# Kernel optimization log

Measured on AMD Instinct MI355X. Metric: run time of the kernel, lower is better.

The kernel has to match this reference:

```python
import jax, jax.numpy as jnp
import numpy as np

B, S, D, H = 4, 2048, 1024, 16
HD = D // H
DFF = 4 * D
NUM_LAYERS = 12
RES = 1.0 / float(np.sqrt(NUM_LAYERS))
SCALE = 1.0 / float(np.sqrt(D))  # module divides by sqrt(embed_dim), not head_dim
EPS = 1e-5


def setup_inputs() -> dict:
    key = jax.random.key(0)
    ks = jax.random.split(key, 12)
    s = 0.02
    p = lambda k, shp: (jax.random.normal(k, shp, jnp.float32) * s)
    return {
        "x": jax.random.normal(ks[0], (B, S, D), jnp.float32),
        "Wq": p(ks[1], (D, D)), "bq": jnp.zeros((D,), jnp.float32),
        "Wk": p(ks[2], (D, D)), "bk": jnp.zeros((D,), jnp.float32),
        "Wv": p(ks[3], (D, D)), "bv": jnp.zeros((D,), jnp.float32),
        "Wo": p(ks[4], (D, D)), "bo": jnp.zeros((D,), jnp.float32),
        "g1": jnp.ones((D,), jnp.float32), "be1": jnp.zeros((D,), jnp.float32),
        "g2": jnp.ones((D,), jnp.float32), "be2": jnp.zeros((D,), jnp.float32),
        "W1": p(ks[5], (D, DFF)), "b1": jnp.zeros((DFF,), jnp.float32),
        "W2": p(ks[6], (DFF, D)), "b2": jnp.zeros((D,), jnp.float32),
    }


def _layernorm(x, g, b):
    m = jnp.mean(x, axis=-1, keepdims=True)
    v = jnp.mean((x - m) ** 2, axis=-1, keepdims=True)
    return (x - m) * jax.lax.rsqrt(v + EPS) * g + b


def _attention(x, Wq, bq, Wk, bk, Wv, bv, Wo, bo):
    b, s, d = x.shape
    q = (x @ Wq + bq).reshape(b, s, H, HD)
    k = (x @ Wk + bk).reshape(b, s, H, HD)
    v = (x @ Wv + bv).reshape(b, s, H, HD)
    scores = jnp.einsum('bqhd,bkhd->bhqk', q, k) * SCALE  # [B,H,S,S]
    mask = jnp.tril(jnp.ones((s, s), dtype=bool))
    scores = jnp.where(mask, scores, -jnp.inf)
    attn = jax.nn.softmax(scores, axis=-1)  # dropout_rate=0 -> identity
    out = jnp.einsum('bhqk,bkhd->bqhd', attn, v).reshape(b, s, d)
    return out @ Wo + bo


def reference(x, Wq, bq, Wk, bk, Wv, bv, Wo, bo, g1, be1, g2, be2, W1, b1, W2, b2):
    x = x + RES * _attention(_layernorm(x, g1, be1), Wq, bq, Wk, bk, Wv, bv, Wo, bo)
    h = _layernorm(x, g2, be2)
    ffn = jax.nn.relu(h @ W1 + b1) @ W2 + b2
    x = x + RES * ffn
    return x
```

## Files before the change

### kernel.cpp

```cpp
#include <hip/hip_runtime.h>

typedef unsigned short ushort_t;
typedef unsigned int uint32;
typedef __attribute__((ext_vector_type(4))) float f32x4;
typedef __attribute__((ext_vector_type(8))) short bf16x8;

#define B_   4
#define S_   2048
#define D_   1024
#define H_   16
#define HD_  64
#define DFF_ 4096
#define M_   (B_ * S_)

#define RES_   0.28867513459481287f
#define SCALE_ 0.03125f
#define EPS_   1e-5f
#define LOG2E_ 1.4426950408889634f

__device__ __forceinline__ ushort_t f2bf(float f) {
    union { float f; uint32 u; } c; c.f = f;
    uint32 u = c.u + 0x7fffu + ((c.u >> 16) & 1u);
    return (ushort_t)(u >> 16);
}
__device__ __forceinline__ float bf2f(ushort_t h) {
    union { uint32 u; float f; } c; c.u = ((uint32)h) << 16;
    return c.f;
}
__device__ __forceinline__ float fexp2(float x) {
    float r; asm("v_exp_f32 %0, %1" : "=v"(r) : "v"(x)); return r;
}
__device__ __forceinline__ uint32 cvt_pk_bf16(float lo, float hi) {
    uint32 r;
    asm("v_cvt_pk_bf16_f32 %0, %1, %2" : "=v"(r) : "v"(lo), "v"(hi));
    return r;
}

#define GLDS(src_, dst_)                                                     \
    __builtin_amdgcn_global_load_lds(                                        \
        (const __attribute__((address_space(1))) void*)(src_),               \
        (__attribute__((address_space(3))) void*)(dst_), 16, 0, 0)

__global__ __launch_bounds__(256) void transpose_cast_kernel(
    const float* __restrict__ W, ushort_t* __restrict__ Wt, int K, int N)
{
    __shared__ float tile[32][33];
    const int bx = blockIdx.x * 32;
    const int by = blockIdx.y * 32;
    const int tx = threadIdx.x;
    const int ty = threadIdx.y;
    #pragma unroll
    for (int i = 0; i < 32; i += 8)
        tile[ty + i][tx] = W[(size_t)(by + ty + i) * N + bx + tx];
    __syncthreads();
    #pragma unroll
    for (int i = 0; i < 32; i += 8)
        Wt[(size_t)(bx + ty + i) * K + by + tx] = f2bf(tile[tx][ty + i]);
}

__global__ void concat_bias_kernel(const float* __restrict__ bq,
                                   const float* __restrict__ bk,
                                   const float* __restrict__ bv,
                                   float* __restrict__ bqkv)
{
    int i = blockIdx.x * blockDim.x + threadIdx.x;
    if (i < 3 * D_) {
        float v = (i < D_) ? bq[i] : (i < 2 * D_) ? bk[i - D_] : bv[i - 2 * D_];
        bqkv[i] = v;
    }
}

__global__ __launch_bounds__(256) void ln_kernel(
    const float* __restrict__ x, const float* __restrict__ g,
    const float* __restrict__ be, ushort_t* __restrict__ out)
{
    const int row = blockIdx.x;
    const int t = threadIdx.x;
    const int lane = t & 63;
    const int wave = t >> 6;
    const float4* xr = (const float4*)(x + (size_t)row * D_);
    float4 v = xr[t];
    float s  = v.x + v.y + v.z + v.w;
    float s2 = v.x * v.x + v.y * v.y + v.z * v.z + v.w * v.w;
    #pragma unroll
    for (int off = 32; off; off >>= 1) {
        s  += __shfl_xor(s, off);
        s2 += __shfl_xor(s2, off);
    }
    __shared__ float red[8];
    if (lane == 0) { red[wave * 2] = s; red[wave * 2 + 1] = s2; }
    __syncthreads();
    s  = red[0] + red[2] + red[4] + red[6];
    s2 = red[1] + red[3] + red[5] + red[7];
    const float mean = s * (1.0f / D_);
    const float var  = s2 * (1.0f / D_) - mean * mean;
    const float rstd = rsqrtf(var + EPS_);
    const float4 gv  = ((const float4*)g)[t];
    const float4 bv  = ((const float4*)be)[t];
    ushort_t o[4];
    o[0] = f2bf((v.x - mean) * rstd * gv.x + bv.x);
    o[1] = f2bf((v.y - mean) * rstd * gv.y + bv.y);
    o[2] = f2bf((v.z - mean) * rstd * gv.z + bv.z);
    o[3] = f2bf((v.w - mean) * rstd * gv.w + bv.w);
    *(ushort2*)&out[(size_t)row * D_ + t * 4]     = make_ushort2(o[0], o[1]);
    *(ushort2*)&out[(size_t)row * D_ + t * 4 + 2] = make_ushort2(o[2], o[3]);
}

template <int MODE, int BM>
__global__ __launch_bounds__(512, (BM == 256) ? 1 : 2) void gemmT_kernel(
    const ushort_t* __restrict__ A, const ushort_t* __restrict__ Bt,
    const float* __restrict__ bias, const float* __restrict__ res,
    void* __restrict__ Cout, int M, int N, int K, int gx)
{
    constexpr int MF     = BM / 32;
    constexpr int ALOADS = BM / 128;
    constexpr int LOADS  = ALOADS + 2;

    __shared__ __align__(16) ushort_t As[3][BM * 32];
    __shared__ __align__(16) ushort_t Bs[3][256 * 32];

    const int tid  = threadIdx.x;
    const int w    = tid >> 6;
    const int lane = tid & 63;
    const int l15  = lane & 15;
    const int g    = lane >> 4;

    const int cpx = gridDim.x >> 3;
    const int swz = (blockIdx.x & 7) * cpx + (blockIdx.x >> 3);
    const int bx = swz % gx, by = swz / gx;
    const int m0 = by * BM, n0 = bx * 256;

    const int wm = (w >> 2) * (BM / 2);
    const int wn = (w & 3) * 64;

    const ushort_t* srcA[ALOADS];
    int ldsA[ALOADS];
    const ushort_t* srcB[2];
    int ldsB[2];
    #pragma unroll
    for (int p = 0; p < ALOADS; ++p) {
        const int L = p * 512 + tid;
        const int row = L >> 2;
        srcA[p] = A + (size_t)(m0 + row) * K + (((L & 3) ^ ((row >> 1) & 3)) << 3);
        ldsA[p] = (p * 512 + w * 64) * 8;
    }
    #pragma unroll
    for (int p = 0; p < 2; ++p) {
        const int L = p * 512 + tid;
        const int row = L >> 2;
        srcB[p] = Bt + (size_t)(n0 + row) * K + (((L & 3) ^ ((row >> 1) & 3)) << 3);
        ldsB[p] = (p * 512 + w * 64) * 8;
    }

    #define STAGE_A(koff_, buf_)                                             \
        do { _Pragma("unroll")                                               \
             for (int p = 0; p < ALOADS; ++p)                                \
                 GLDS(srcA[p] + (koff_), &As[buf_][ldsA[p]]); } while (0)
    #define STAGE_B(koff_, buf_)                                             \
        do { _Pragma("unroll")                                               \
             for (int p = 0; p < 2; ++p)                                     \
                 GLDS(srcB[p] + (koff_), &Bs[buf_][ldsB[p]]); } while (0)

    #define LDA(mf_) (*(const bf16x8*)&As[cur][(wm + (mf_) * 16 + l15) * 32 + \
                        ((g ^ (((wm + (mf_) * 16 + l15) >> 1) & 3)) << 3)])
    #define LDB(nf_) (*(const bf16x8*)&Bs[cur][(wn + (nf_) * 16 + l15) * 32 + \
                        ((g ^ (((wn + (nf_) * 16 + l15) >> 1) & 3)) << 3)])

    f32x4 acc[MF][4] = {};
    const int NT = K >> 5;

    STAGE_A(0, 0); STAGE_B(0, 0);
    STAGE_A(32, 1); STAGE_B(32, 1);
    asm volatile("s_waitcnt vmcnt(%0)" :: "n"(LOADS) : "memory");
    __builtin_amdgcn_s_barrier();

    for (int t = 0; t < NT; ++t) {
        const int cur = t % 3;
        const int nb  = (t + 2) % 3;
        const bool more = (t + 2 < NT);
        const size_t koff = (size_t)(t + 2) * 32;

        bf16x8 af[4], bfr[4];
        #pragma unroll
        for (int nf = 0; nf < 4; ++nf) bfr[nf] = LDB(nf);
        #pragma unroll
        for (int mf = 0; mf < 4; ++mf) af[mf] = LDA(mf);

        if (BM == 256) {
            if (more) STAGE_A(koff, nb);
            __builtin_amdgcn_s_barrier();
            __builtin_amdgcn_s_setprio(1);
            #pragma unroll
            for (int mf = 0; mf < 4; ++mf)
                #pragma unroll
                for (int nf = 0; nf < 4; ++nf)
                    acc[mf][nf] = __builtin_amdgcn_mfma_f32_16x16x32_bf16(
                        af[mf], bfr[nf], acc[mf][nf], 0, 0, 0);
            __builtin_amdgcn_s_setprio(0);
            __builtin_amdgcn_s_barrier();

            #pragma unroll
            for (int mf = 0; mf < 4; ++mf) af[mf] = LDA(mf + 4);
            if (more) STAGE_B(koff, nb);
            __builtin_amdgcn_s_barrier();
            __builtin_amdgcn_s_setprio(1);
            #pragma unroll
            for (int mf = 0; mf < 4; ++mf)
                #pragma unroll
                for (int nf = 0; nf < 4; ++nf)
                    acc[(MF == 8 ? mf + 4 : mf)][nf] =
                        __builtin_amdgcn_mfma_f32_16x16x32_bf16(
                            af[mf], bfr[nf], acc[(MF == 8 ? mf + 4 : mf)][nf], 0, 0, 0);
            __builtin_amdgcn_s_setprio(0);
            if (more)
                asm volatile("s_waitcnt vmcnt(%0)" :: "n"(LOADS) : "memory");
            else
                asm volatile("s_waitcnt vmcnt(0)" ::: "memory");
            __builtin_amdgcn_s_barrier();
        } else {
            if (more) { STAGE_A(koff, nb); STAGE_B(koff, nb); }
            __builtin_amdgcn_s_setprio(1);
            #pragma unroll
            for (int mf = 0; mf < 4; ++mf)
                #pragma unroll
                for (int nf = 0; nf < 4; ++nf)
                    acc[mf][nf] = __builtin_amdgcn_mfma_f32_16x16x32_bf16(
                        af[mf], bfr[nf], acc[mf][nf], 0, 0, 0);
            __builtin_amdgcn_s_setprio(0);
            if (more)
                asm volatile("s_waitcnt vmcnt(%0)" :: "n"(LOADS) : "memory");
            else
                asm volatile("s_waitcnt vmcnt(0)" ::: "memory");
            __builtin_amdgcn_s_barrier();
        }
    }
    #undef STAGE_A
    #undef STAGE_B
    #undef LDA
    #undef LDB

    const int rbase = g * 4;
    #pragma unroll
    for (int mf = 0; mf < MF; ++mf) {
        #pragma unroll
        for (int nf = 0; nf < 4; ++nf) {
            const int col = n0 + wn + nf * 16 + l15;
            const float bcol = bias[col];
            #pragma unroll
            for (int r = 0; r < 4; ++r) {
                const int row = m0 + wm + mf * 16 + rbase + r;
                float v = acc[mf][nf][r] + bcol;
                const size_t idx = (size_t)row * N + col;
                if (MODE == 0) {
                    ((ushort_t*)Cout)[idx] = f2bf(v);
                } else if (MODE == 1) {
                    ((ushort_t*)Cout)[idx] = f2bf(fmaxf(v, 0.0f));
                } else {
                    ((float*)Cout)[idx] = res[idx] + RES_ * v;
                }
            }
        }
    }
}

__global__ __launch_bounds__(256) void fattn_kernel(
    const ushort_t* __restrict__ qkv, ushort_t* __restrict__ out)
{
    __shared__ __align__(16) ushort_t Ks[64 * 64];
    __shared__ __align__(16) ushort_t Vt[64 * 64];
    __shared__ __align__(16) ushort_t Ps[4][16 * 64];

    const int tid  = threadIdx.x;
    const int lane = tid & 63;
    const int w    = tid >> 6;
    const int bh = blockIdx.y;
    const int b = bh >> 4, h = bh & 15;

    const int l15 = lane & 15;
    const int g   = lane >> 4;

    const size_t rs = 3 * D_;
    const ushort_t* Qg = qkv + (size_t)b * S_ * rs + h * HD_;
    const ushort_t* Kg = Qg + D_;

    const int skey = tid >> 3;
    const int sc   = tid & 7;

    #pragma unroll
    for (int half = 0; half < 2; ++half) {
        const int qt = half ? blockIdx.x : (S_ / 64 - 1) - blockIdx.x;
        const int q0 = qt * 64;
        const int nkb = qt + 1;

        bf16x8 qf[2];
        {
            const int qrow = q0 + w * 16 + l15;
            #pragma unroll
            for (int kk = 0; kk < 2; ++kk) {
                bf16x8 tq = *(const bf16x8*)(Qg + (size_t)qrow * rs + kk * 32 + g * 8);
                #pragma unroll
                for (int e = 0; e < 8; ++e)
                    tq[e] = (short)f2bf(bf2f((ushort_t)tq[e]) * (SCALE_ * LOG2E_));
                qf[kk] = tq;
            }
        }

        float mrow = -1e30f, lrow = 0.f;
        f32x4 oacc[4] = {};

        bf16x8 kvreg[2], vvreg[2];
        #pragma unroll
        for (int pass = 0; pass < 2; ++pass) {
            const ushort_t* src = Kg + (size_t)(pass * 32 + skey) * rs + sc * 8;
            kvreg[pass] = *(const bf16x8*)src;
            vvreg[pass] = *(const bf16x8*)(src + D_);
        }

        for (int kb = 0; kb < nkb; ++kb) {
            __syncthreads();
            #pragma unroll
            for (int pass = 0; pass < 2; ++pass) {
                const int key = pass * 32 + skey;
                *(bf16x8*)&Ks[key * 64 + ((sc ^ (key & 7)) << 3)] = kvreg[pass];
                #pragma unroll
                for (int j = 0; j < 8; ++j) {
                    const int d  = sc * 8 + j;
                    const int cp = (key >> 3) ^ (d & 7) ^ ((d >> 3) & 7);
                    Vt[d * 64 + (cp << 3) + (key & 7)] = (ushort_t)vvreg[pass][j];
                }
            }
            if (kb + 1 < nkb) {
                #pragma unroll
                for (int pass = 0; pass < 2; ++pass) {
                    const ushort_t* src =
                        Kg + (size_t)((kb + 1) * 64 + pass * 32 + skey) * rs + sc * 8;
                    kvreg[pass] = *(const bf16x8*)src;
                    vvreg[pass] = *(const bf16x8*)(src + D_);
                }
            }
            __syncthreads();

            f32x4 sf[4] = {};
            __builtin_amdgcn_s_setprio(1);
            #pragma unroll
            for (int kk = 0; kk < 2; ++kk) {
                const int cc = kk * 4 + g;
                #pragma unroll
                for (int nf = 0; nf < 4; ++nf) {
                    const int keyr = nf * 16 + l15;
                    bf16x8 kf = *(const bf16x8*)&Ks[keyr * 64 + ((cc ^ (keyr & 7)) << 3)];
                    sf[nf] = __builtin_amdgcn_mfma_f32_16x16x32_bf16(kf, qf[kk], sf[nf], 0, 0, 0);
                }
            }
            __builtin_amdgcn_s_setprio(0);

            if (kb == nkb - 1) {
                const int q = q0 + w * 16 + l15;
                #pragma unroll
                for (int nf = 0; nf < 4; ++nf)
                    #pragma unroll
                    for (int r = 0; r < 4; ++r)
                        if (kb * 64 + nf * 16 + g * 4 + r > q) sf[nf][r] = -1e30f;
            }
            float mx = -1e30f;
            #pragma unroll
            for (int nf = 0; nf < 4; ++nf)
                #pragma unroll
                for (int r = 0; r < 4; ++r) mx = fmaxf(mx, sf[nf][r]);
            mx = fmaxf(mx, __shfl_xor(mx, 16));
            mx = fmaxf(mx, __shfl_xor(mx, 32));

            if (!__all(mx - mrow <= 8.0f)) {
                const float mnew = fmaxf(mrow, mx);
                const float corr = fexp2(mrow - mnew);
                mrow = mnew;
                lrow *= corr;
                #pragma unroll
                for (int r = 0; r < 4; ++r) {
                    const float cr = __shfl(corr, g * 4 + r, 16);
                    #pragma unroll
                    for (int nf = 0; nf < 4; ++nf) oacc[nf][r] *= cr;
                }
            }

            {
                const int qrow = l15;
                float psum = 0.f;
                #pragma unroll
                for (int nf = 0; nf < 4; ++nf) {
                    const float p0 = fexp2(sf[nf][0] - mrow);
                    const float p1 = fexp2(sf[nf][1] - mrow);
                    const float p2 = fexp2(sf[nf][2] - mrow);
                    const float p3 = fexp2(sf[nf][3] - mrow);
                    psum += (p0 + p1) + (p2 + p3);
                    uint2 pk = make_uint2(cvt_pk_bf16(p0, p1), cvt_pk_bf16(p2, p3));
                    const int c16 = ((nf << 1) + (g >> 1)) ^ (qrow & 7);
                    *(uint2*)((char*)Ps[w] + qrow * 128 + c16 * 16 + (g & 1) * 8) = pk;
                }
                psum += __shfl_xor(psum, 16);
                psum += __shfl_xor(psum, 32);
                lrow += psum;
            }

            #pragma unroll
            for (int kk = 0; kk < 2; ++kk) {
                const int cc = kk * 4 + g;
                const int qrow = l15;
                const int c16 = cc ^ (qrow & 7);
                bf16x8 pa = *(const bf16x8*)((const char*)Ps[w] + qrow * 128 + c16 * 16);
                __builtin_amdgcn_s_setprio(1);
                #pragma unroll
                for (int nf = 0; nf < 4; ++nf) {
                    const int dr  = nf * 16 + l15;
                    const int cvp = cc ^ (dr & 7) ^ ((dr >> 3) & 7);
                    bf16x8 vf = *(const bf16x8*)&Vt[dr * 64 + (cvp << 3)];
                    oacc[nf] = __builtin_amdgcn_mfma_f32_16x16x32_bf16(pa, vf, oacc[nf], 0, 0, 0);
                }
                __builtin_amdgcn_s_setprio(0);
            }
        }

        const float linv = 1.0f / lrow;
        #pragma unroll
        for (int r = 0; r < 4; ++r) {
            const float li = __shfl(linv, g * 4 + r, 16);
            const int q = q0 + w * 16 + g * 4 + r;
            ushort_t* op = out + (size_t)(b * S_ + q) * D_ + h * HD_;
            #pragma unroll
            for (int nf = 0; nf < 4; ++nf)
                op[nf * 16 + l15] = f2bf(oacc[nf][r] * li);
        }
    }
}

extern "C" void kernel_launch(void* const* d_in, const int* in_sizes, int n_in,
                              void* d_out, int out_size, void* d_ws, size_t ws_size,
                              hipStream_t stream)
{
    const float* x   = (const float*)d_in[0];
    const float* Wq  = (const float*)d_in[1];
    const float* bq  = (const float*)d_in[2];
    const float* Wk  = (const float*)d_in[3];
    const float* bk  = (const float*)d_in[4];
    const float* Wv  = (const float*)d_in[5];
    const float* bv  = (const float*)d_in[6];
    const float* Wo  = (const float*)d_in[7];
    const float* bo  = (const float*)d_in[8];
    const float* g1  = (const float*)d_in[9];
    const float* be1 = (const float*)d_in[10];
    const float* g2  = (const float*)d_in[11];
    const float* be2 = (const float*)d_in[12];
    const float* W1  = (const float*)d_in[13];
    const float* b1  = (const float*)d_in[14];
    const float* W2  = (const float*)d_in[15];
    const float* b2  = (const float*)d_in[16];
    float* out = (float*)d_out;

    char* ws = (char*)d_ws;
    size_t o = 0;
    auto alloc = [&](size_t bytes) { size_t r = o; o = (o + bytes + 255) & ~(size_t)255; return r; };
    ushort_t* Wqkvt = (ushort_t*)(ws + alloc((size_t)3 * D_ * D_ * 2));
    ushort_t* Wot   = (ushort_t*)(ws + alloc((size_t)D_ * D_ * 2));
    ushort_t* W1t   = (ushort_t*)(ws + alloc((size_t)DFF_ * D_ * 2));
    ushort_t* W2t   = (ushort_t*)(ws + alloc((size_t)D_ * DFF_ * 2));
    float*    bqkv  = (float*)(ws + alloc((size_t)3 * D_ * 4));
    ushort_t* lnbuf = (ushort_t*)(ws + alloc((size_t)M_ * D_ * 2));
    ushort_t* bigbuf= (ushort_t*)(ws + alloc((size_t)M_ * DFF_ * 2));
    ushort_t* attnb = (ushort_t*)(ws + alloc((size_t)M_ * D_ * 2));
    float*    x1    = (float*)(ws + alloc((size_t)M_ * D_ * 4));

    dim3 tblock(32, 8);
    transpose_cast_kernel<<<dim3(D_/32, D_/32), tblock, 0, stream>>>(Wq, Wqkvt,            D_, D_);
    transpose_cast_kernel<<<dim3(D_/32, D_/32), tblock, 0, stream>>>(Wk, Wqkvt + D_*D_,    D_, D_);
    transpose_cast_kernel<<<dim3(D_/32, D_/32), tblock, 0, stream>>>(Wv, Wqkvt + 2*D_*D_,  D_, D_);
    transpose_cast_kernel<<<dim3(D_/32, D_/32), tblock, 0, stream>>>(Wo, Wot,              D_, D_);
    transpose_cast_kernel<<<dim3(DFF_/32, D_/32), tblock, 0, stream>>>(W1, W1t,            D_, DFF_);
    transpose_cast_kernel<<<dim3(D_/32, DFF_/32), tblock, 0, stream>>>(W2, W2t,            DFF_, D_);
    concat_bias_kernel<<<12, 256, 0, stream>>>(bq, bk, bv, bqkv);

    ln_kernel<<<M_, 256, 0, stream>>>(x, g1, be1, lnbuf);
    gemmT_kernel<0, 256><<<(M_/256)*(3*D_/256), 512, 0, stream>>>(
        lnbuf, Wqkvt, bqkv, nullptr, bigbuf, M_, 3*D_, D_, 3*D_/256);
    fattn_kernel<<<dim3(S_/128, B_*H_), 256, 0, stream>>>(bigbuf, attnb);
    gemmT_kernel<2, 128><<<(M_/128)*(D_/256), 512, 0, stream>>>(
        attnb, Wot, bo, x, x1, M_, D_, D_, D_/256);
    ln_kernel<<<M_, 256, 0, stream>>>(x1, g2, be2, lnbuf);
    gemmT_kernel<1, 256><<<(M_/256)*(DFF_/256), 512, 0, stream>>>(
        lnbuf, W1t, b1, nullptr, bigbuf, M_, DFF_, D_, DFF_/256);
    gemmT_kernel<2, 128><<<(M_/128)*(D_/256), 512, 0, stream>>>(
        bigbuf, W2t, b2, x1, out, M_, D_, DFF_, D_/256);
}
```

Measured before the change: 388.2 us.

## Write V transposed from QKV GEMM epilogue, drop in-kernel V transpose in attention

The QKV GEMM gets a new mode that writes the V columns straight into a per-(batch,head) transposed [HD, S] buffer. The attention kernel then loads V^T rows with vector loads and stores them to shared memory with 16-byte swizzled writes, replacing the per-element scalar transpose scatter. The attention grid is also flattened to 1D with the head index varying fastest. The cost is strided 8-byte stores in the GEMM epilogue and an extra workspace buffer.

```diff
diff --git a/kernel.cpp b/kernel.cpp
--- a/kernel.cpp
+++ b/kernel.cpp
@@ -110,7 +110,8 @@
 __global__ __launch_bounds__(512, (BM == 256) ? 1 : 2) void gemmT_kernel(
     const ushort_t* __restrict__ A, const ushort_t* __restrict__ Bt,
     const float* __restrict__ bias, const float* __restrict__ res,
-    void* __restrict__ Cout, int M, int N, int K, int gx)
+    void* __restrict__ Cout, ushort_t* __restrict__ vt,
+    int M, int N, int K, int gx)
 {
     constexpr int MF     = BM / 32;
     constexpr int ALOADS = BM / 128;
@@ -240,23 +241,34 @@
     #undef LDB
 
     const int rbase = g * 4;
+    const bool isV = (MODE == 3) && (n0 >= 2 * D_);
     #pragma unroll
     for (int mf = 0; mf < MF; ++mf) {
         #pragma unroll
         for (int nf = 0; nf < 4; ++nf) {
             const int col = n0 + wn + nf * 16 + l15;
             const float bcol = bias[col];
-            #pragma unroll
-            for (int r = 0; r < 4; ++r) {
-                const int row = m0 + wm + mf * 16 + rbase + r;
-                float v = acc[mf][nf][r] + bcol;
-                const size_t idx = (size_t)row * N + col;
-                if (MODE == 0) {
-                    ((ushort_t*)Cout)[idx] = f2bf(v);
-                } else if (MODE == 1) {
-                    ((ushort_t*)Cout)[idx] = f2bf(fmaxf(v, 0.0f));
-                } else {
-                    ((float*)Cout)[idx] = res[idx] + RES_ * v;
+            if (isV) {
+                const int d  = col - 2 * D_;
+                const int b  = m0 >> 11;
+                const int sb = (m0 + wm + mf * 16 + rbase) & (S_ - 1);
+                ushort4 pk = make_ushort4(
+                    f2bf(acc[mf][nf][0] + bcol), f2bf(acc[mf][nf][1] + bcol),
+                    f2bf(acc[mf][nf][2] + bcol), f2bf(acc[mf][nf][3] + bcol));
+                *(ushort4*)&vt[(((size_t)(b * H_ + (d >> 6)) * HD_) + (d & 63)) * S_ + sb] = pk;
+            } else {
+                #pragma unroll
+                for (int r = 0; r < 4; ++r) {
+                    const int row = m0 + wm + mf * 16 + rbase + r;
+                    float v = acc[mf][nf][r] + bcol;
+                    const size_t idx = (size_t)row * N + col;
+                    if (MODE == 0 || MODE == 3) {
+                        ((ushort_t*)Cout)[idx] = f2bf(v);
+                    } else if (MODE == 1) {
+                        ((ushort_t*)Cout)[idx] = f2bf(fmaxf(v, 0.0f));
+                    } else {
+                        ((float*)Cout)[idx] = res[idx] + RES_ * v;
+                    }
                 }
             }
         }
@@ -264,7 +276,8 @@
 }
 
 __global__ __launch_bounds__(256) void fattn_kernel(
-    const ushort_t* __restrict__ qkv, ushort_t* __restrict__ out)
+    const ushort_t* __restrict__ qkv, const ushort_t* __restrict__ vtg,
+    ushort_t* __restrict__ out)
 {
     __shared__ __align__(16) ushort_t Ks[64 * 64];
     __shared__ __align__(16) ushort_t Vt[64 * 64];
@@ -273,7 +286,9 @@
     const int tid  = threadIdx.x;
     const int lane = tid & 63;
     const int w    = tid >> 6;
-    const int bh = blockIdx.y;
+    const int lin  = blockIdx.x;
+    const int xi   = lin >> 6;
+    const int bh   = lin & 63;
     const int b = bh >> 4, h = bh & 15;
 
     const int l15 = lane & 15;
@@ -282,13 +297,14 @@
     const size_t rs = 3 * D_;
     const ushort_t* Qg = qkv + (size_t)b * S_ * rs + h * HD_;
     const ushort_t* Kg = Qg + D_;
-
-    const int skey = tid >> 3;
+    const ushort_t* Vg = vtg + (size_t)bh * HD_ * S_;
+
+    const int srow = tid >> 3;
     const int sc   = tid & 7;
 
     #pragma unroll
     for (int half = 0; half < 2; ++half) {
-        const int qt = half ? blockIdx.x : (S_ / 64 - 1) - blockIdx.x;
+        const int qt = half ? xi : (S_ / 64 - 1) - xi;
         const int q0 = qt * 64;
         const int nkb = qt + 1;
 
@@ -311,31 +327,27 @@
         bf16x8 kvreg[2], vvreg[2];
         #pragma unroll
         for (int pass = 0; pass < 2; ++pass) {
-            const ushort_t* src = Kg + (size_t)(pass * 32 + skey) * rs + sc * 8;
-            kvreg[pass] = *(const bf16x8*)src;
-            vvreg[pass] = *(const bf16x8*)(src + D_);
+            const int row = pass * 32 + srow;
+            kvreg[pass] = *(const bf16x8*)(Kg + (size_t)row * rs + sc * 8);
+            vvreg[pass] = *(const bf16x8*)(Vg + (size_t)row * S_ + sc * 8);
         }
 
         for (int kb = 0; kb < nkb; ++kb) {
             __syncthreads();
             #pragma unroll
             for (int pass = 0; pass < 2; ++pass) {
-                const int key = pass * 32 + skey;
-                *(bf16x8*)&Ks[key * 64 + ((sc ^ (key & 7)) << 3)] = kvreg[pass];
-                #pragma unroll
-                for (int j = 0; j < 8; ++j) {
-                    const int d  = sc * 8 + j;
-                    const int cp = (key >> 3) ^ (d & 7) ^ ((d >> 3) & 7);
-                    Vt[d * 64 + (cp << 3) + (key & 7)] = (ushort_t)vvreg[pass][j];
-                }
+                const int row = pass * 32 + srow;
+                *(bf16x8*)&Ks[row * 64 + ((sc ^ (row & 7)) << 3)] = kvreg[pass];
+                *(bf16x8*)&Vt[row * 64 + ((sc ^ (row & 7)) << 3)] = vvreg[pass];
             }
             if (kb + 1 < nkb) {
                 #pragma unroll
                 for (int pass = 0; pass < 2; ++pass) {
-                    const ushort_t* src =
-                        Kg + (size_t)((kb + 1) * 64 + pass * 32 + skey) * rs + sc * 8;
-                    kvreg[pass] = *(const bf16x8*)src;
-                    vvreg[pass] = *(const bf16x8*)(src + D_);
+                    const int row = pass * 32 + srow;
+                    kvreg[pass] = *(const bf16x8*)(
+                        Kg + (size_t)((kb + 1) * 64 + row) * rs + sc * 8);
+                    vvreg[pass] = *(const bf16x8*)(
+                        Vg + (size_t)row * S_ + (kb + 1) * 64 + sc * 8);
                 }
             }
             __syncthreads();
@@ -411,9 +423,8 @@
                 __builtin_amdgcn_s_setprio(1);
                 #pragma unroll
                 for (int nf = 0; nf < 4; ++nf) {
-                    const int dr  = nf * 16 + l15;
-                    const int cvp = cc ^ (dr & 7) ^ ((dr >> 3) & 7);
-                    bf16x8 vf = *(const bf16x8*)&Vt[dr * 64 + (cvp << 3)];
+                    const int dr = nf * 16 + l15;
+                    bf16x8 vf = *(const bf16x8*)&Vt[dr * 64 + ((cc ^ (dr & 7)) << 3)];
                     oacc[nf] = __builtin_amdgcn_mfma_f32_16x16x32_bf16(pa, vf, oacc[nf], 0, 0, 0);
                 }
                 __builtin_amdgcn_s_setprio(0);
@@ -468,6 +479,7 @@
     ushort_t* bigbuf= (ushort_t*)(ws + alloc((size_t)M_ * DFF_ * 2));
     ushort_t* attnb = (ushort_t*)(ws + alloc((size_t)M_ * D_ * 2));
     float*    x1    = (float*)(ws + alloc((size_t)M_ * D_ * 4));
+    ushort_t* vtbuf = (ushort_t*)(ws + alloc((size_t)M_ * D_ * 2));
 
     dim3 tblock(32, 8);
     transpose_cast_kernel<<<dim3(D_/32, D_/32), tblock, 0, stream>>>(Wq, Wqkvt,            D_, D_);
@@ -479,14 +491,14 @@
     concat_bias_kernel<<<12, 256, 0, stream>>>(bq, bk, bv, bqkv);
 
     ln_kernel<<<M_, 256, 0, stream>>>(x, g1, be1, lnbuf);
-    gemmT_kernel<0, 256><<<(M_/256)*(3*D_/256), 512, 0, stream>>>(
-        lnbuf, Wqkvt, bqkv, nullptr, bigbuf, M_, 3*D_, D_, 3*D_/256);
-    fattn_kernel<<<dim3(S_/128, B_*H_), 256, 0, stream>>>(bigbuf, attnb);
+    gemmT_kernel<3, 256><<<(M_/256)*(3*D_/256), 512, 0, stream>>>(
+        lnbuf, Wqkvt, bqkv, nullptr, bigbuf, vtbuf, M_, 3*D_, D_, 3*D_/256);
+    fattn_kernel<<<(S_/128) * 64, 256, 0, stream>>>(bigbuf, vtbuf, attnb);
     gemmT_kernel<2, 128><<<(M_/128)*(D_/256), 512, 0, stream>>>(
-        attnb, Wot, bo, x, x1, M_, D_, D_, D_/256);
+        attnb, Wot, bo, x, x1, nullptr, M_, D_, D_, D_/256);
     ln_kernel<<<M_, 256, 0, stream>>>(x1, g2, be2, lnbuf);
     gemmT_kernel<1, 256><<<(M_/256)*(DFF_/256), 512, 0, stream>>>(
-        lnbuf, W1t, b1, nullptr, bigbuf, M_, DFF_, D_, DFF_/256);
+        lnbuf, W1t, b1, nullptr, bigbuf, nullptr, M_, DFF_, D_, DFF_/256);
     gemmT_kernel<2, 128><<<(M_/128)*(D_/256), 512, 0, stream>>>(
-        bigbuf, W2t, b2, x1, out, M_, D_, DFF_, D_/256);
-}
+        bigbuf, W2t, b2, x1, out, nullptr, M_, D_, DFF_, D_/256);
+}
```

After: 382.9 us. No clear change (-1.4%).

## Pre-transpose V, process two key blocks per attention step, unify GEMM to 128-row tiles

Applied to the files above, without the earlier changes.

Adds a separate kernel that transposes V into a per-head [HD, S] buffer, so the attention kernel can stage V with vector stores instead of scalar scattered LDS writes. The attention loop now processes two 64-key blocks per iteration with double-buffered K/V in shared memory and one online-softmax update per pair, and blocks are launched on a flattened 1D grid. The GEMM drops the 256-row tile variant, so QKV and FFN1 use 128-row tiles with 2 blocks per CU. The costs are an extra kernel launch, an extra workspace buffer and more global traffic for V, along with higher register pressure in the attention kernel.

```diff
diff --git a/kernel.cpp b/kernel.cpp
--- a/kernel.cpp
+++ b/kernel.cpp
@@ -106,17 +106,47 @@
     *(ushort2*)&out[(size_t)row * D_ + t * 4 + 2] = make_ushort2(o[2], o[3]);
 }
 
-template <int MODE, int BM>
-__global__ __launch_bounds__(512, (BM == 256) ? 1 : 2) void gemmT_kernel(
+__global__ __launch_bounds__(256) void vtrans_kernel(
+    const ushort_t* __restrict__ qkv, ushort_t* __restrict__ vt)
+{
+    __shared__ __align__(16) ushort_t T[256 * 64];
+    const int tid  = threadIdx.x;
+    const int sblk = blockIdx.x & 7;
+    const int bh   = blockIdx.x >> 3;
+    const int b = bh >> 4, h = bh & 15;
+    const ushort_t* src = qkv + (size_t)(b * S_ + sblk * 256) * (3 * D_) + 2 * D_ + h * 64;
+    #pragma unroll
+    for (int p = 0; p < 8; ++p) {
+        const int L = p * 256 + tid;
+        const int s = L >> 3, c = L & 7;
+        bf16x8 v = *(const bf16x8*)(src + (size_t)s * (3 * D_) + c * 8);
+        *(bf16x8*)&T[s * 64 + ((c ^ (s & 7)) << 3)] = v;
+    }
+    __syncthreads();
+    #pragma unroll
+    for (int p = 0; p < 8; ++p) {
+        const int L = p * 256 + tid;
+        const int hd = L >> 5, scn = L & 31;
+        ushort_t tmp[8];
+        #pragma unroll
+        for (int j = 0; j < 8; ++j) {
+            const int s = scn * 8 + j;
+            tmp[j] = T[s * 64 + (((hd >> 3) ^ (s & 7)) << 3) + (hd & 7)];
+        }
+        *(bf16x8*)&vt[((size_t)bh * 64 + hd) * S_ + sblk * 256 + scn * 8] =
+            *(const bf16x8*)tmp;
+    }
+}
+
+template <int MODE>
+__global__ __launch_bounds__(512, 2) void gemmT_kernel(
     const ushort_t* __restrict__ A, const ushort_t* __restrict__ Bt,
     const float* __restrict__ bias, const float* __restrict__ res,
     void* __restrict__ Cout, int M, int N, int K, int gx)
 {
-    constexpr int MF     = BM / 32;
-    constexpr int ALOADS = BM / 128;
-    constexpr int LOADS  = ALOADS + 2;
-
-    __shared__ __align__(16) ushort_t As[3][BM * 32];
+    constexpr int LOADS = 3;
+
+    __shared__ __align__(16) ushort_t As[3][128 * 32];
     __shared__ __align__(16) ushort_t Bs[3][256 * 32];
 
     const int tid  = threadIdx.x;
@@ -128,21 +158,20 @@
     const int cpx = gridDim.x >> 3;
     const int swz = (blockIdx.x & 7) * cpx + (blockIdx.x >> 3);
     const int bx = swz % gx, by = swz / gx;
-    const int m0 = by * BM, n0 = bx * 256;
-
-    const int wm = (w >> 2) * (BM / 2);
+    const int m0 = by * 128, n0 = bx * 256;
+
+    const int wm = (w >> 2) * 64;
     const int wn = (w & 3) * 64;
 
-    const ushort_t* srcA[ALOADS];
-    int ldsA[ALOADS];
+    const ushort_t* srcA;
+    int ldsA;
     const ushort_t* srcB[2];
     int ldsB[2];
-    #pragma unroll
-    for (int p = 0; p < ALOADS; ++p) {
-        const int L = p * 512 + tid;
+    {
+        const int L = tid;
         const int row = L >> 2;
-        srcA[p] = A + (size_t)(m0 + row) * K + (((L & 3) ^ ((row >> 1) & 3)) << 3);
-        ldsA[p] = (p * 512 + w * 64) * 8;
+        srcA = A + (size_t)(m0 + row) * K + (((L & 3) ^ ((row >> 1) & 3)) << 3);
+        ldsA = (w * 64) * 8;
     }
     #pragma unroll
     for (int p = 0; p < 2; ++p) {
@@ -152,31 +181,28 @@
         ldsB[p] = (p * 512 + w * 64) * 8;
     }
 
-    #define STAGE_A(koff_, buf_)                                             \
-        do { _Pragma("unroll")                                               \
-             for (int p = 0; p < ALOADS; ++p)                                \
-                 GLDS(srcA[p] + (koff_), &As[buf_][ldsA[p]]); } while (0)
-    #define STAGE_B(koff_, buf_)                                             \
-        do { _Pragma("unroll")                                               \
-             for (int p = 0; p < 2; ++p)                                     \
-                 GLDS(srcB[p] + (koff_), &Bs[buf_][ldsB[p]]); } while (0)
+    #define STAGE(koff_, buf_)                                               \
+        do {                                                                 \
+            GLDS(srcA + (koff_), &As[buf_][ldsA]);                           \
+            GLDS(srcB[0] + (koff_), &Bs[buf_][ldsB[0]]);                     \
+            GLDS(srcB[1] + (koff_), &Bs[buf_][ldsB[1]]);                     \
+        } while (0)
 
     #define LDA(mf_) (*(const bf16x8*)&As[cur][(wm + (mf_) * 16 + l15) * 32 + \
                         ((g ^ (((wm + (mf_) * 16 + l15) >> 1) & 3)) << 3)])
     #define LDB(nf_) (*(const bf16x8*)&Bs[cur][(wn + (nf_) * 16 + l15) * 32 + \
                         ((g ^ (((wn + (nf_) * 16 + l15) >> 1) & 3)) << 3)])
 
-    f32x4 acc[MF][4] = {};
+    f32x4 acc[4][4] = {};
     const int NT = K >> 5;
 
-    STAGE_A(0, 0); STAGE_B(0, 0);
-    STAGE_A(32, 1); STAGE_B(32, 1);
+    STAGE(0, 0);
+    STAGE(32, 1);
     asm volatile("s_waitcnt vmcnt(%0)" :: "n"(LOADS) : "memory");
     __builtin_amdgcn_s_barrier();
 
     for (int t = 0; t < NT; ++t) {
         const int cur = t % 3;
-        const int nb  = (t + 2) % 3;
         const bool more = (t + 2 < NT);
         const size_t koff = (size_t)(t + 2) * 32;
 
@@ -186,62 +212,28 @@
         #pragma unroll
         for (int mf = 0; mf < 4; ++mf) af[mf] = LDA(mf);
 
-        if (BM == 256) {
-            if (more) STAGE_A(koff, nb);
-            __builtin_amdgcn_s_barrier();
-            __builtin_amdgcn_s_setprio(1);
-            #pragma unroll
-            for (int mf = 0; mf < 4; ++mf)
-                #pragma unroll
-                for (int nf = 0; nf < 4; ++nf)
-                    acc[mf][nf] = __builtin_amdgcn_mfma_f32_16x16x32_bf16(
-                        af[mf], bfr[nf], acc[mf][nf], 0, 0, 0);
-            __builtin_amdgcn_s_setprio(0);
-            __builtin_amdgcn_s_barrier();
-
-            #pragma unroll
-            for (int mf = 0; mf < 4; ++mf) af[mf] = LDA(mf + 4);
-            if (more) STAGE_B(koff, nb);
-            __builtin_amdgcn_s_barrier();
-            __builtin_amdgcn_s_setprio(1);
-            #pragma unroll
-            for (int mf = 0; mf < 4; ++mf)
-                #pragma unroll
-                for (int nf = 0; nf < 4; ++nf)
-                    acc[(MF == 8 ? mf + 4 : mf)][nf] =
-                        __builtin_amdgcn_mfma_f32_16x16x32_bf16(
-                            af[mf], bfr[nf], acc[(MF == 8 ? mf + 4 : mf)][nf], 0, 0, 0);
-            __builtin_amdgcn_s_setprio(0);
-            if (more)
-                asm volatile("s_waitcnt vmcnt(%0)" :: "n"(LOADS) : "memory");
-            else
-                asm volatile("s_waitcnt vmcnt(0)" ::: "memory");
-            __builtin_amdgcn_s_barrier();
-        } else {
-            if (more) { STAGE_A(koff, nb); STAGE_B(koff, nb); }
-            __builtin_amdgcn_s_setprio(1);
-            #pragma unroll
-            for (int mf = 0; mf < 4; ++mf)
-                #pragma unroll
-                for (int nf = 0; nf < 4; ++nf)
-                    acc[mf][nf] = __builtin_amdgcn_mfma_f32_16x16x32_bf16(
-                        af[mf], bfr[nf], acc[mf][nf], 0, 0, 0);
-            __builtin_amdgcn_s_setprio(0);
-            if (more)
-                asm volatile("s_waitcnt vmcnt(%0)" :: "n"(LOADS) : "memory");
-            else
-                asm volatile("s_waitcnt vmcnt(0)" ::: "memory");
-            __builtin_amdgcn_s_barrier();
-        }
-    }
-    #undef STAGE_A
-    #undef STAGE_B
+        if (more) STAGE(koff, (t + 2) % 3);
+        __builtin_amdgcn_s_setprio(1);
+        #pragma unroll
+        for (int mf = 0; mf < 4; ++mf)
+            #pragma unroll
+            for (int nf = 0; nf < 4; ++nf)
+                acc[mf][nf] = __builtin_amdgcn_mfma_f32_16x16x32_bf16(
+                    af[mf], bfr[nf], acc[mf][nf], 0, 0, 0);
+        __builtin_amdgcn_s_setprio(0);
+        if (more)
+            asm volatile("s_waitcnt vmcnt(%0)" :: "n"(LOADS) : "memory");
+        else
+            asm volatile("s_waitcnt vmcnt(0)" ::: "memory");
+        __builtin_amdgcn_s_barrier();
+    }
+    #undef STAGE
     #undef LDA
     #undef LDB
 
     const int rbase = g * 4;
     #pragma unroll
-    for (int mf = 0; mf < MF; ++mf) {
+    for (int mf = 0; mf < 4; ++mf) {
         #pragma unroll
         for (int nf = 0; nf < 4; ++nf) {
             const int col = n0 + wn + nf * 16 + l15;
@@ -264,16 +256,19 @@
 }
 
 __global__ __launch_bounds__(256) void fattn_kernel(
-    const ushort_t* __restrict__ qkv, ushort_t* __restrict__ out)
-{
-    __shared__ __align__(16) ushort_t Ks[64 * 64];
-    __shared__ __align__(16) ushort_t Vt[64 * 64];
+    const ushort_t* __restrict__ qkv, const ushort_t* __restrict__ vtg,
+    ushort_t* __restrict__ out)
+{
+    __shared__ __align__(16) ushort_t Ks[2][64 * 64];
+    __shared__ __align__(16) ushort_t Vt[2][64 * 64];
     __shared__ __align__(16) ushort_t Ps[4][16 * 64];
 
     const int tid  = threadIdx.x;
     const int lane = tid & 63;
     const int w    = tid >> 6;
-    const int bh = blockIdx.y;
+    const int lin  = blockIdx.x;
+    const int xi   = lin >> 6;
+    const int bh   = lin & 63;
     const int b = bh >> 4, h = bh & 15;
 
     const int l15 = lane & 15;
@@ -282,13 +277,14 @@
     const size_t rs = 3 * D_;
     const ushort_t* Qg = qkv + (size_t)b * S_ * rs + h * HD_;
     const ushort_t* Kg = Qg + D_;
-
-    const int skey = tid >> 3;
+    const ushort_t* Vg = vtg + (size_t)bh * HD_ * S_;
+
+    const int srow = tid >> 3;
     const int sc   = tid & 7;
 
     #pragma unroll
     for (int half = 0; half < 2; ++half) {
-        const int qt = half ? blockIdx.x : (S_ / 64 - 1) - blockIdx.x;
+        const int qt = half ? xi : (S_ / 64 - 1) - xi;
         const int q0 = qt * 64;
         const int nkb = qt + 1;
 
@@ -308,39 +304,56 @@
         float mrow = -1e30f, lrow = 0.f;
         f32x4 oacc[4] = {};
 
-        bf16x8 kvreg[2], vvreg[2];
-        #pragma unroll
-        for (int pass = 0; pass < 2; ++pass) {
-            const ushort_t* src = Kg + (size_t)(pass * 32 + skey) * rs + sc * 8;
-            kvreg[pass] = *(const bf16x8*)src;
-            vvreg[pass] = *(const bf16x8*)(src + D_);
-        }
-
-        for (int kb = 0; kb < nkb; ++kb) {
+        bf16x8 kvreg[2][2], vvreg[2][2];
+        #pragma unroll
+        for (int p = 0; p < 2; ++p) {
+            const int row = p * 32 + srow;
+            kvreg[0][p] = *(const bf16x8*)(Kg + (size_t)row * rs + sc * 8);
+            vvreg[0][p] = *(const bf16x8*)(Vg + (size_t)row * S_ + sc * 8);
+        }
+        if (nkb > 1) {
+            #pragma unroll
+            for (int p = 0; p < 2; ++p) {
+                const int row = p * 32 + srow;
+                kvreg[1][p] = *(const bf16x8*)(Kg + (size_t)(64 + row) * rs + sc * 8);
+                vvreg[1][p] = *(const bf16x8*)(Vg + (size_t)row * S_ + 64 + sc * 8);
+            }
+        }
+
+        int kb = 0;
+        for (; kb + 1 < nkb; kb += 2) {
             __syncthreads();
             #pragma unroll
-            for (int pass = 0; pass < 2; ++pass) {
-                const int key = pass * 32 + skey;
-                *(bf16x8*)&Ks[key * 64 + ((sc ^ (key & 7)) << 3)] = kvreg[pass];
-                #pragma unroll
-                for (int j = 0; j < 8; ++j) {
-                    const int d  = sc * 8 + j;
-                    const int cp = (key >> 3) ^ (d & 7) ^ ((d >> 3) & 7);
-                    Vt[d * 64 + (cp << 3) + (key & 7)] = (ushort_t)vvreg[pass][j];
-                }
-            }
-            if (kb + 1 < nkb) {
-                #pragma unroll
-                for (int pass = 0; pass < 2; ++pass) {
-                    const ushort_t* src =
-                        Kg + (size_t)((kb + 1) * 64 + pass * 32 + skey) * rs + sc * 8;
-                    kvreg[pass] = *(const bf16x8*)src;
-                    vvreg[pass] = *(const bf16x8*)(src + D_);
+            for (int s = 0; s < 2; ++s)
+                #pragma unroll
+                for (int p = 0; p < 2; ++p) {
+                    const int row = p * 32 + srow;
+                    *(bf16x8*)&Ks[s][row * 64 + ((sc ^ (row & 7)) << 3)] = kvreg[s][p];
+                    *(bf16x8*)&Vt[s][row * 64 + ((sc ^ (row & 7)) << 3)] = vvreg[s][p];
+                }
+            if (kb + 2 < nkb) {
+                #pragma unroll
+                for (int p = 0; p < 2; ++p) {
+                    const int row = p * 32 + srow;
+                    kvreg[0][p] = *(const bf16x8*)(
+                        Kg + (size_t)((kb + 2) * 64 + row) * rs + sc * 8);
+                    vvreg[0][p] = *(const bf16x8*)(
+                        Vg + (size_t)row * S_ + (kb + 2) * 64 + sc * 8);
+                }
+            }
+            if (kb + 3 < nkb) {
+                #pragma unroll
+                for (int p = 0; p < 2; ++p) {
+                    const int row = p * 32 + srow;
+                    kvreg[1][p] = *(const bf16x8*)(
+                        Kg + (size_t)((kb + 3) * 64 + row) * rs + sc * 8);
+                    vvreg[1][p] = *(const bf16x8*)(
+                        Vg + (size_t)row * S_ + (kb + 3) * 64 + sc * 8);
                 }
             }
             __syncthreads();
 
-            f32x4 sf[4] = {};
+            f32x4 sf0[4] = {}, sf1[4] = {};
             __builtin_amdgcn_s_setprio(1);
             #pragma unroll
             for (int kk = 0; kk < 2; ++kk) {
@@ -348,25 +361,32 @@
                 #pragma unroll
                 for (int nf = 0; nf < 4; ++nf) {
                     const int keyr = nf * 16 + l15;
-                    bf16x8 kf = *(const bf16x8*)&Ks[keyr * 64 + ((cc ^ (keyr & 7)) << 3)];
-                    sf[nf] = __builtin_amdgcn_mfma_f32_16x16x32_bf16(kf, qf[kk], sf[nf], 0, 0, 0);
+                    const int ko = keyr * 64 + ((cc ^ (keyr & 7)) << 3);
+                    bf16x8 kf0 = *(const bf16x8*)&Ks[0][ko];
+                    bf16x8 kf1 = *(const bf16x8*)&Ks[1][ko];
+                    sf0[nf] = __builtin_amdgcn_mfma_f32_16x16x32_bf16(kf0, qf[kk], sf0[nf], 0, 0, 0);
+                    sf1[nf] = __builtin_amdgcn_mfma_f32_16x16x32_bf16(kf1, qf[kk], sf1[nf], 0, 0, 0);
                 }
             }
             __builtin_amdgcn_s_setprio(0);
 
-            if (kb == nkb - 1) {
+            if (kb + 1 == nkb - 1) {
                 const int q = q0 + w * 16 + l15;
                 #pragma unroll
                 for (int nf = 0; nf < 4; ++nf)
                     #pragma unroll
                     for (int r = 0; r < 4; ++r)
-                        if (kb * 64 + nf * 16 + g * 4 + r > q) sf[nf][r] = -1e30f;
-            }
+                        if ((kb + 1) * 64 + nf * 16 + g * 4 + r > q) sf1[nf][r] = -1e30f;
+            }
+
             float mx = -1e30f;
             #pragma unroll
             for (int nf = 0; nf < 4; ++nf)
                 #pragma unroll
-                for (int r = 0; r < 4; ++r) mx = fmaxf(mx, sf[nf][r]);
+                for (int r = 0; r < 4; ++r) {
+                    mx = fmaxf(mx, sf0[nf][r]);
+                    mx = fmaxf(mx, sf1[nf][r]);
+                }
             mx = fmaxf(mx, __shfl_xor(mx, 16));
             mx = fmaxf(mx, __shfl_xor(mx, 32));
 
@@ -383,37 +403,122 @@
                 }
             }
 
-            {
-                const int qrow = l15;
-                float psum = 0.f;
+            float psum = 0.f;
+            const int qrow = l15;
+            #pragma unroll
+            for (int s = 0; s < 2; ++s) {
+                const f32x4* sfp = s ? sf1 : sf0;
                 #pragma unroll
                 for (int nf = 0; nf < 4; ++nf) {
-                    const float p0 = fexp2(sf[nf][0] - mrow);
-                    const float p1 = fexp2(sf[nf][1] - mrow);
-                    const float p2 = fexp2(sf[nf][2] - mrow);
-                    const float p3 = fexp2(sf[nf][3] - mrow);
+                    const float p0 = fexp2(sfp[nf][0] - mrow);
+                    const float p1 = fexp2(sfp[nf][1] - mrow);
+                    const float p2 = fexp2(sfp[nf][2] - mrow);
+                    const float p3 = fexp2(sfp[nf][3] - mrow);
                     psum += (p0 + p1) + (p2 + p3);
                     uint2 pk = make_uint2(cvt_pk_bf16(p0, p1), cvt_pk_bf16(p2, p3));
                     const int c16 = ((nf << 1) + (g >> 1)) ^ (qrow & 7);
                     *(uint2*)((char*)Ps[w] + qrow * 128 + c16 * 16 + (g & 1) * 8) = pk;
                 }
-                psum += __shfl_xor(psum, 16);
-                psum += __shfl_xor(psum, 32);
-                lrow += psum;
-            }
-
+                #pragma unroll
+                for (int kk = 0; kk < 2; ++kk) {
+                    const int cc = kk * 4 + g;
+                    const int c16 = cc ^ (qrow & 7);
+                    bf16x8 pa = *(const bf16x8*)((const char*)Ps[w] + qrow * 128 + c16 * 16);
+                    __builtin_amdgcn_s_setprio(1);
+                    #pragma unroll
+                    for (int nf = 0; nf < 4; ++nf) {
+                        const int dr = nf * 16 + l15;
+                        bf16x8 vf = *(const bf16x8*)&Vt[s][dr * 64 + ((cc ^ (dr & 7)) << 3)];
+                        oacc[nf] = __builtin_amdgcn_mfma_f32_16x16x32_bf16(pa, vf, oacc[nf], 0, 0, 0);
+                    }
+                    __builtin_amdgcn_s_setprio(0);
+                }
+            }
+            psum += __shfl_xor(psum, 16);
+            psum += __shfl_xor(psum, 32);
+            lrow += psum;
+        }
+
+        if (kb < nkb) {
+            __syncthreads();
+            #pragma unroll
+            for (int p = 0; p < 2; ++p) {
+                const int row = p * 32 + srow;
+                *(bf16x8*)&Ks[0][row * 64 + ((sc ^ (row & 7)) << 3)] = kvreg[0][p];
+                *(bf16x8*)&Vt[0][row * 64 + ((sc ^ (row & 7)) << 3)] = vvreg[0][p];
+            }
+            __syncthreads();
+
+            f32x4 sf0[4] = {};
+            __builtin_amdgcn_s_setprio(1);
             #pragma unroll
             for (int kk = 0; kk < 2; ++kk) {
                 const int cc = kk * 4 + g;
-                const int qrow = l15;
+                #pragma unroll
+                for (int nf = 0; nf < 4; ++nf) {
+                    const int keyr = nf * 16 + l15;
+                    bf16x8 kf = *(const bf16x8*)&Ks[0][keyr * 64 + ((cc ^ (keyr & 7)) << 3)];
+                    sf0[nf] = __builtin_amdgcn_mfma_f32_16x16x32_bf16(kf, qf[kk], sf0[nf], 0, 0, 0);
+                }
+            }
+            __builtin_amdgcn_s_setprio(0);
+
+            {
+                const int q = q0 + w * 16 + l15;
+                #pragma unroll
+                for (int nf = 0; nf < 4; ++nf)
+                    #pragma unroll
+                    for (int r = 0; r < 4; ++r)
+                        if (kb * 64 + nf * 16 + g * 4 + r > q) sf0[nf][r] = -1e30f;
+            }
+            float mx = -1e30f;
+            #pragma unroll
+            for (int nf = 0; nf < 4; ++nf)
+                #pragma unroll
+                for (int r = 0; r < 4; ++r) mx = fmaxf(mx, sf0[nf][r]);
+            mx = fmaxf(mx, __shfl_xor(mx, 16));
+            mx = fmaxf(mx, __shfl_xor(mx, 32));
+
+            if (!__all(mx - mrow <= 8.0f)) {
+                const float mnew = fmaxf(mrow, mx);
+                const float corr = fexp2(mrow - mnew);
+                mrow = mnew;
+                lrow *= corr;
+                #pragma unroll
+                for (int r = 0; r < 4; ++r) {
+                    const float cr = __shfl(corr, g * 4 + r, 16);
+                    #pragma unroll
+                    for (int nf = 0; nf < 4; ++nf) oacc[nf][r] *= cr;
+                }
+            }
+
+            float psum = 0.f;
+            const int qrow = l15;
+            #pragma unroll
+            for (int nf = 0; nf < 4; ++nf) {
+                const float p0 = fexp2(sf0[nf][0] - mrow);
+                const float p1 = fexp2(sf0[nf][1] - mrow);
+                const float p2 = fexp2(sf0[nf][2] - mrow);
+                const float p3 = fexp2(sf0[nf][3] - mrow);
+                psum += (p0 + p1) + (p2 + p3);
+                uint2 pk = make_uint2(cvt_pk_bf16(p0, p1), cvt_pk_bf16(p2, p3));
+                const int c16 = ((nf << 1) + (g >> 1)) ^ (qrow & 7);
+                *(uint2*)((char*)Ps[w] + qrow * 128 + c16 * 16 + (g & 1) * 8) = pk;
+            }
+            psum += __shfl_xor(psum, 16);
+            psum += __shfl_xor(psum, 32);
+            lrow += psum;
+
+            #pragma unroll
+            for (int kk = 0; kk < 2; ++kk) {
+                const int cc = kk * 4 + g;
                 const int c16 = cc ^ (qrow & 7);
                 bf16x8 pa = *(const bf16x8*)((const char*)Ps[w] + qrow * 128 + c16 * 16);
                 __builtin_amdgcn_s_setprio(1);
                 #pragma unroll
                 for (int nf = 0; nf < 4; ++nf) {
-                    const int dr  = nf * 16 + l15;
-                    const int cvp = cc ^ (dr & 7) ^ ((dr >> 3) & 7);
-                    bf16x8 vf = *(const bf16x8*)&Vt[dr * 64 + (cvp << 3)];
+                    const int dr = nf * 16 + l15;
+                    bf16x8 vf = *(const bf16x8*)&Vt[0][dr * 64 + ((cc ^ (dr & 7)) << 3)];
                     oacc[nf] = __builtin_amdgcn_mfma_f32_16x16x32_bf16(pa, vf, oacc[nf], 0, 0, 0);
                 }
                 __builtin_amdgcn_s_setprio(0);
@@ -468,6 +573,7 @@
     ushort_t* bigbuf= (ushort_t*)(ws + alloc((size_t)M_ * DFF_ * 2));
     ushort_t* attnb = (ushort_t*)(ws + alloc((size_t)M_ * D_ * 2));
     float*    x1    = (float*)(ws + alloc((size_t)M_ * D_ * 4));
+    ushort_t* vtbuf = (ushort_t*)(ws + alloc((size_t)M_ * D_ * 2));
 
     dim3 tblock(32, 8);
     transpose_cast_kernel<<<dim3(D_/32, D_/32), tblock, 0, stream>>>(Wq, Wqkvt,            D_, D_);
@@ -479,14 +585,15 @@
     concat_bias_kernel<<<12, 256, 0, stream>>>(bq, bk, bv, bqkv);
 
     ln_kernel<<<M_, 256, 0, stream>>>(x, g1, be1, lnbuf);
-    gemmT_kernel<0, 256><<<(M_/256)*(3*D_/256), 512, 0, stream>>>(
+    gemmT_kernel<0><<<(M_/128)*(3*D_/256), 512, 0, stream>>>(
         lnbuf, Wqkvt, bqkv, nullptr, bigbuf, M_, 3*D_, D_, 3*D_/256);
-    fattn_kernel<<<dim3(S_/128, B_*H_), 256, 0, stream>>>(bigbuf, attnb);
-    gemmT_kernel<2, 128><<<(M_/128)*(D_/256), 512, 0, stream>>>(
+    vtrans_kernel<<<512, 256, 0, stream>>>(bigbuf, vtbuf);
+    fattn_kernel<<<(S_/128) * 64, 256, 0, stream>>>(bigbuf, vtbuf, attnb);
+    gemmT_kernel<2><<<(M_/128)*(D_/256), 512, 0, stream>>>(
         attnb, Wot, bo, x, x1, M_, D_, D_, D_/256);
     ln_kernel<<<M_, 256, 0, stream>>>(x1, g2, be2, lnbuf);
-    gemmT_kernel<1, 256><<<(M_/256)*(DFF_/256), 512, 0, stream>>>(
+    gemmT_kernel<1><<<(M_/128)*(DFF_/256), 512, 0, stream>>>(
         lnbuf, W1t, b1, nullptr, bigbuf, M_, DFF_, D_, DFF_/256);
-    gemmT_kernel<2, 128><<<(M_/128)*(D_/256), 512, 0, stream>>>(
+    gemmT_kernel<2><<<(M_/128)*(D_/256), 512, 0, stream>>>(
         bigbuf, W2t, b2, x1, out, M_, D_, DFF_, D_/256);
 }
```

Measured after the change: 381.4 us. About the same (-1.7%).
